# Kernel tuning notes

Hardware: AMD Instinct MI355X
Metric: run time of the kernel (lower is better)

## Reference

```python
import math
import jax, jax.numpy as jnp
import numpy as np

EPS = 1e-5
NUM_HEADER = 2


def pos_encoding(C, T, dtype):
    i = jnp.arange(C)
    exp = -((i - (i % 2)).astype(dtype) / C)
    freqs = jnp.power(jnp.asarray(10000.0, dtype), exp)[:, None]      # [C,1]
    phases = ((i % 2).astype(dtype) * (np.pi / 2))[:, None]           # [C,1]
    pos = jnp.arange(T, dtype=dtype)[None, :]                         # [1,T]
    return jnp.sin(pos * freqs + phases)                              # [C,T]


def layernorm2d(x, g, b):
    # LayerNorm over (C,T) jointly, per batch element (nn.LayerNorm([C, length]))
    mu = jnp.mean(x, axis=(1, 2), keepdims=True)
    var = jnp.mean((x - mu) ** 2, axis=(1, 2), keepdims=True)
    return (x - mu) * jax.lax.rsqrt(var + EPS) * g[None] + b[None]


def dsconv(x, dw_w, dw_b, pw_w, pw_b):
    # depthwise conv1d (groups=C, 'same' padding for odd k) + pointwise 1x1
    C = x.shape[1]
    k = dw_w.shape[-1]
    y = jax.lax.conv_general_dilated(
        x, dw_w[:, None, :], (1,), [(k // 2, k // 2)],
        dimension_numbers=('NCH', 'OIH', 'NCH'), feature_group_count=C)
    y = y + dw_b[None, :, None]
    y = jnp.einsum('bct,oc->bot', y, pw_w) + pw_b[None, :, None]
    return y


def attention(x, mask, Wq, Wk, Wv, Wo):
    # Faithful to source bug: all heads use Wqs[1]/Wks[1]/Wvs[1] -> identical heads.
    xt = jnp.transpose(x, (0, 2, 1))          # [B,T,C]
    C = xt.shape[-1]
    dk = C / NUM_HEADER
    q = xt @ Wq                               # [B,T,dk]
    k_ = xt @ Wk
    v = xt @ Wv
    s = jnp.einsum('bqd,bkd->bqk', q, k_) * (1.0 / math.sqrt(dk))
    hmask = mask[:, None, :]                  # mask over keys
    s = s * hmask + (1 - hmask) * (-1e30)
    a = jax.nn.softmax(s, axis=2) * mask[:, :, None]
    head = a @ v                              # [B,T,dk]
    heads = jnp.tile(head, (1, 1, NUM_HEADER))  # concat of identical heads
    out = heads @ Wo                          # [B,T,C]
    return jnp.transpose(out, (0, 2, 1))      # [B,C,T]


def setup_inputs() -> dict:
    key = jax.random.key(0)
    B, C, T = 16, 128, 1024
    NCONV, K = 4, 7
    dk = C // NUM_HEADER
    ks = jax.random.split(key, 12)
    inp = {
        'x': jax.random.normal(ks[0], (B, C, T), jnp.float32),
        'mask': jnp.ones((B, T), jnp.float32),
        'dw_w': jax.random.normal(ks[1], (NCONV, C, K), jnp.float32) * math.sqrt(2.0 / K),
        'dw_b': jnp.zeros((NCONV, C), jnp.float32),
        'pw_w': jax.random.normal(ks[2], (NCONV, C, C), jnp.float32) * math.sqrt(2.0 / C),
        'pw_b': jnp.zeros((NCONV, C), jnp.float32),
        'norm0_g': jnp.ones((C, T), jnp.float32),
        'norm0_b': jnp.zeros((C, T), jnp.float32),
        'norms_g': jnp.ones((NCONV, C, T), jnp.float32),
        'norms_b': jnp.zeros((NCONV, C, T), jnp.float32),
        'norme_g': jnp.ones((C, T), jnp.float32),
        'norme_b': jnp.zeros((C, T), jnp.float32),
        'Wq': jax.random.normal(ks[3], (C, dk), jnp.float32) * math.sqrt(2.0 / (C + dk)),
        'Wk': jax.random.normal(ks[4], (C, dk), jnp.float32) * math.sqrt(2.0 / (C + dk)),
        'Wv': jax.random.normal(ks[5], (C, dk), jnp.float32) * math.sqrt(2.0 / (C + dk)),
        'Wo': jax.random.normal(ks[6], (C, C), jnp.float32) * math.sqrt(2.0 / C),
        'fc_w': jax.random.normal(ks[7], (C, C), jnp.float32) * (0.1 * math.sqrt(6.0 / (2 * C))),
        'fc_b': jnp.zeros((C,), jnp.float32),
    }
    return inp


def reference(x, mask, dw_w, dw_b, pw_w, pw_b, norm0_g, norm0_b,
              norms_g, norms_b, norme_g, norme_b,
              Wq, Wk, Wv, Wo, fc_w, fc_b):
    B, C, T = x.shape
    nconv = dw_w.shape[0]
    # dropout is identity in eval mode (reference is deterministic)
    out = x + pos_encoding(C, T, x.dtype)[None]
    res = layernorm2d(out, norm0_g, norm0_b)
    for i in range(nconv):
        out = dsconv(out, dw_w[i], dw_b[i], pw_w[i], pw_b[i])
        out = jax.nn.relu(out)
        out = out + res
        res = out
        out = layernorm2d(out, norms_g[i], norms_b[i])
    out = attention(out, mask, Wq, Wk, Wv, Wo)
    out = out + res
    res = out
    out = layernorm2d(out, norme_g, norme_b)
    out = jnp.einsum('bct,oc->bot', out, fc_w) + fc_b[None, :, None]
    out = jax.nn.relu(out)
    out = out + res
    return out
```

## Files before the change

kernel.cpp:

```cpp
#include <hip/hip_runtime.h>
#include <math.h>

#define BB 16
#define CC 128
#define TT 1024
#define KK 7
#define DK 64
#define NSPLIT 4

typedef float f32x4 __attribute__((ext_vector_type(4)));
typedef short s16x8 __attribute__((ext_vector_type(8)));

__device__ inline short f2bf(float f) {
  union { float f; unsigned u; } v; v.f = f;
  unsigned r = (v.u + 0x7FFFu + ((v.u >> 16) & 1u)) >> 16;
  return (short)r;
}

__device__ inline float bf2f(short s) {
  union { unsigned u; float f; } v;
  v.u = ((unsigned)(unsigned short)s) << 16;
  return v.f;
}

__device__ inline void block_partial_256(float s, float ss, float* dst) {
#pragma unroll
  for (int off = 32; off; off >>= 1) { s += __shfl_xor(s, off); ss += __shfl_xor(ss, off); }
  __shared__ float red[8];
  int w = threadIdx.x >> 6;
  if ((threadIdx.x & 63) == 0) { red[2 * w] = s; red[2 * w + 1] = ss; }
  __syncthreads();
  if (threadIdx.x == 0) {
    for (int i = 1; i < 4; ++i) { s += red[2 * i]; ss += red[2 * i + 1]; }
    dst[0] = s; dst[1] = ss;
  }
}

__device__ inline void ln_stats_from_parts(const float* part_batch, int n, float* sh) {
  if (threadIdx.x < 64) {
    float s = 0.f, ss = 0.f;
    for (int i = threadIdx.x; i < n; i += 64) { s += part_batch[2 * i]; ss += part_batch[2 * i + 1]; }
#pragma unroll
    for (int off = 32; off; off >>= 1) { s += __shfl_xor(s, off); ss += __shfl_xor(ss, off); }
    if (threadIdx.x == 0) {
      const float invN = 1.f / (float)(CC * TT);
      float mu = s * invN;
      sh[0] = mu;
      sh[1] = rsqrtf(ss * invN - mu * mu + 1e-5f);
    }
  }
  __syncthreads();
}

__global__ __launch_bounds__(256) void k_prep0(const float* __restrict__ pww,
                                               const float* __restrict__ Wq,
                                               const float* __restrict__ Wk,
                                               const float* __restrict__ Wv,
                                               const float* __restrict__ Wo,
                                               const float* __restrict__ fcw,
                                               const float* __restrict__ x,
                                               short* __restrict__ pwwb,
                                               short* __restrict__ wqkvb,
                                               short* __restrict__ wo2b,
                                               short* __restrict__ fcwb,
                                               float* __restrict__ part0) {
  if (blockIdx.x < 448) {
    int i = blockIdx.x * 256 + threadIdx.x;
    if (i < 65536) { pwwb[i] = f2bf(pww[i]); return; }
    i -= 65536;
    if (i < 24576) {
      int m = i >> 7, c = i & 127;
      int sel = m >> 6, d = m & 63;
      const float* srcp = sel == 0 ? Wq : (sel == 1 ? Wk : Wv);
      wqkvb[i] = f2bf(srcp[c * DK + d]);
      return;
    }
    i -= 24576;
    if (i < 8192) {
      int o = i >> 6, d = i & 63;
      wo2b[i] = f2bf(Wo[d * CC + o] + Wo[(d + 64) * CC + o]);
      return;
    }
    i -= 8192;
    fcwb[i] = f2bf(fcw[i]);
    return;
  }
  int w = threadIdx.x >> 6, lane = threadIdx.x & 63;
  int bc = (blockIdx.x - 448) * 4 + w;
  int c = bc & (CC - 1);
  float freq = expf(-((float)(c & ~1) * (1.f / (float)CC)) * 9.210340371976184f);
  float ph = (c & 1) ? 1.5707963267948966f : 0.f;
  const float* xr = x + (size_t)bc * TT;
  float s = 0.f, ss = 0.f;
#pragma unroll
  for (int k = 0; k < 4; ++k) {
    int t = (k * 64 + lane) * 4;
    float4 v = *(const float4*)(xr + t);
    v.x += sinf((float)(t + 0) * freq + ph);
    v.y += sinf((float)(t + 1) * freq + ph);
    v.z += sinf((float)(t + 2) * freq + ph);
    v.w += sinf((float)(t + 3) * freq + ph);
    s += v.x + v.y + v.z + v.w;
    ss += v.x * v.x + v.y * v.y + v.z * v.z + v.w * v.w;
  }
#pragma unroll
  for (int off = 32; off; off >>= 1) { s += __shfl_xor(s, off); ss += __shfl_xor(ss, off); }
  if (lane == 0) { part0[(size_t)bc * 2] = s; part0[(size_t)bc * 2 + 1] = ss; }
}

template <bool LN_IN, bool LN_RES, bool ADD_POS>
__global__ __launch_bounds__(256) void k_dsconv(const float* __restrict__ in,
                                                const float* __restrict__ lng,
                                                const float* __restrict__ lnb,
                                                const float* __restrict__ part_in, int npart,
                                                const float* __restrict__ dww,
                                                const float* __restrict__ dwb,
                                                const short* __restrict__ pwwb,
                                                const float* __restrict__ pwb,
                                                float* __restrict__ out,
                                                float* __restrict__ part_out) {
  int tile = blockIdx.x & 31, b = blockIdx.x >> 5;
  int t0 = tile * 32;
  __shared__ float stats[2];
  __shared__ float xs[CC][41];
  __shared__ float xr2[CC][33];
  __shared__ __align__(16) short Dt[32][136];
  ln_stats_from_parts(part_in + (size_t)b * npart * 2, npart, stats);
  float mu = stats[0], rs = stats[1];

  for (int i = threadIdx.x; i < CC * 10; i += 256) {
    int c = i / 10, q = i - c * 10;
    int tb = t0 - 4 + q * 4;
    const float* rowp = in + ((size_t)b * CC + c) * TT;
    float freq = 0.f, ph = 0.f;
    if (ADD_POS) {
      freq = expf(-((float)(c & ~1) * (1.f / (float)CC)) * 9.210340371976184f);
      ph = (c & 1) ? 1.5707963267948966f : 0.f;
    }
    float r0, r1, r2, r3, o0, o1, o2, o3;
    bool full = (tb >= 0) && (tb + 4 <= TT);
    if (full) {
      float4 v = *(const float4*)(rowp + tb);
      if (ADD_POS) {
        v.x += sinf((float)(tb + 0) * freq + ph);
        v.y += sinf((float)(tb + 1) * freq + ph);
        v.z += sinf((float)(tb + 2) * freq + ph);
        v.w += sinf((float)(tb + 3) * freq + ph);
      }
      r0 = v.x; r1 = v.y; r2 = v.z; r3 = v.w;
      o0 = r0; o1 = r1; o2 = r2; o3 = r3;
      if (LN_IN) {
        float4 g = *(const float4*)(lng + (size_t)c * TT + tb);
        float4 bv = *(const float4*)(lnb + (size_t)c * TT + tb);
        o0 = (r0 - mu) * rs * g.x + bv.x;
        o1 = (r1 - mu) * rs * g.y + bv.y;
        o2 = (r2 - mu) * rs * g.z + bv.z;
        o3 = (r3 - mu) * rs * g.w + bv.w;
      }
    } else {
      float rr[4], oo[4];
#pragma unroll
      for (int k = 0; k < 4; ++k) {
        int t = tb + k;
        bool inb = (t >= 0) && (t < TT);
        float rv = 0.f;
        if (inb) {
          rv = rowp[t];
          if (ADD_POS) rv += sinf((float)t * freq + ph);
        }
        rr[k] = rv;
        float ov = rv;
        if (LN_IN && inb)
          ov = (rv - mu) * rs * lng[(size_t)c * TT + t] + lnb[(size_t)c * TT + t];
        oo[k] = ov;
      }
      r0 = rr[0]; r1 = rr[1]; r2 = rr[2]; r3 = rr[3];
      o0 = oo[0]; o1 = oo[1]; o2 = oo[2]; o3 = oo[3];
    }
    if (LN_IN && q >= 1 && q <= 8) {
      int tl = (q - 1) * 4;
      xr2[c][tl] = r0; xr2[c][tl + 1] = r1; xr2[c][tl + 2] = r2; xr2[c][tl + 3] = r3;
    }
    int base = q * 4;
    xs[c][base] = o0; xs[c][base + 1] = o1; xs[c][base + 2] = o2; xs[c][base + 3] = o3;
  }
  __syncthreads();
  for (int i = threadIdx.x; i < 32 * CC; i += 256) {
    int t = i >> 7, c = i & 127;
    float a = dwb[c];
#pragma unroll
    for (int j = 0; j < KK; ++j) a += dww[c * KK + j] * xs[c][t + j + 1];
    Dt[t][c] = f2bf(a);
  }
  __syncthreads();

  int w = threadIdx.x >> 6, lane = threadIdx.x & 63;
  int lo = lane & 15, hi = lane >> 4;
  f32x4 acc[2][2];
#pragma unroll
  for (int mt = 0; mt < 2; ++mt)
#pragma unroll
    for (int nt = 0; nt < 2; ++nt) { acc[mt][nt][0] = 0.f; acc[mt][nt][1] = 0.f; acc[mt][nt][2] = 0.f; acc[mt][nt][3] = 0.f; }
#pragma unroll
  for (int ks = 0; ks < 4; ++ks) {
    s16x8 b0 = *(const s16x8*)&Dt[lo][ks * 32 + hi * 8];
    s16x8 b1 = *(const s16x8*)&Dt[16 + lo][ks * 32 + hi * 8];
    s16x8 a0 = *(const s16x8*)&pwwb[(size_t)(w * 32 + lo) * CC + ks * 32 + hi * 8];
    s16x8 a1 = *(const s16x8*)&pwwb[(size_t)(w * 32 + 16 + lo) * CC + ks * 32 + hi * 8];
    acc[0][0] = __builtin_amdgcn_mfma_f32_16x16x32_bf16(a0, b0, acc[0][0], 0, 0, 0);
    acc[0][1] = __builtin_amdgcn_mfma_f32_16x16x32_bf16(a0, b1, acc[0][1], 0, 0, 0);
    acc[1][0] = __builtin_amdgcn_mfma_f32_16x16x32_bf16(a1, b0, acc[1][0], 0, 0, 0);
    acc[1][1] = __builtin_amdgcn_mfma_f32_16x16x32_bf16(a1, b1, acc[1][1], 0, 0, 0);
  }

  float s = 0.f, ss = 0.f;
#pragma unroll
  for (int mt = 0; mt < 2; ++mt)
#pragma unroll
    for (int nt = 0; nt < 2; ++nt)
#pragma unroll
      for (int r = 0; r < 4; ++r) {
        int row = w * 32 + mt * 16 + hi * 4 + r;
        int tl = nt * 16 + lo;
        int t = t0 + tl;
        float v = acc[mt][nt][r] + pwb[row];
        v = v > 0.f ? v : 0.f;
        float rv;
        if (LN_RES) {
          float raw = xs[row][tl + 4];
          rv = (raw - mu) * rs * lng[row * TT + t] + lnb[row * TT + t];
        } else if (LN_IN) {
          rv = xr2[row][tl];
        } else {
          rv = xs[row][tl + 4];
        }
        v += rv;
        xr2[row][tl] = v;
        s += v; ss += v * v;
      }
  __syncthreads();
  for (int u = threadIdx.x; u < 1024; u += 256) {
    int c = u >> 3, q = u & 7;
    float4 o4;
    o4.x = xr2[c][q * 4]; o4.y = xr2[c][q * 4 + 1];
    o4.z = xr2[c][q * 4 + 2]; o4.w = xr2[c][q * 4 + 3];
    *(float4*)(out + ((size_t)b * CC + c) * TT + t0 + q * 4) = o4;
  }
  block_partial_256(s, ss, part_out + (size_t)blockIdx.x * 2);
}

__global__ __launch_bounds__(256) void k_qkv(const float* __restrict__ in,
                                             const float* __restrict__ lng,
                                             const float* __restrict__ lnb,
                                             const float* __restrict__ part_in,
                                             const short* __restrict__ wqkvb,
                                             short* __restrict__ q,
                                             short* __restrict__ k,
                                             short* __restrict__ vt) {
  int tile = blockIdx.x & 31, b = blockIdx.x >> 5;
  int t0 = tile * 32;
  __shared__ float stats[2];
  __shared__ __align__(16) short Dt[32][136];
  __shared__ __align__(16) short stgQ[32 * 64];
  __shared__ __align__(16) short stgK[32 * 64];
  __shared__ __align__(16) short stgV[64][40];
  ln_stats_from_parts(part_in + (size_t)b * 64, 32, stats);
  float mu = stats[0], rs = stats[1];
  for (int i = threadIdx.x; i < CC * 8; i += 256) {
    int c = i >> 3, qq = i & 7;
    int t = qq * 4;
    size_t off = (size_t)c * TT + t0 + t;
    float4 v = *(const float4*)(in + (size_t)b * CC * TT + off);
    float4 g = *(const float4*)(lng + off);
    float4 bb = *(const float4*)(lnb + off);
    Dt[t + 0][c] = f2bf((v.x - mu) * rs * g.x + bb.x);
    Dt[t + 1][c] = f2bf((v.y - mu) * rs * g.y + bb.y);
    Dt[t + 2][c] = f2bf((v.z - mu) * rs * g.z + bb.z);
    Dt[t + 3][c] = f2bf((v.w - mu) * rs * g.w + bb.w);
  }
  __syncthreads();

  int w = threadIdx.x >> 6, lane = threadIdx.x & 63;
  int lo = lane & 15, hi = lane >> 4;
  f32x4 acc[3][2];
#pragma unroll
  for (int mt = 0; mt < 3; ++mt)
#pragma unroll
    for (int nt = 0; nt < 2; ++nt) { acc[mt][nt][0] = 0.f; acc[mt][nt][1] = 0.f; acc[mt][nt][2] = 0.f; acc[mt][nt][3] = 0.f; }
#pragma unroll
  for (int ks = 0; ks < 4; ++ks) {
    s16x8 b0 = *(const s16x8*)&Dt[lo][ks * 32 + hi * 8];
    s16x8 b1 = *(const s16x8*)&Dt[16 + lo][ks * 32 + hi * 8];
#pragma unroll
    for (int mt = 0; mt < 3; ++mt) {
      s16x8 a = *(const s16x8*)&wqkvb[(size_t)(w * 48 + mt * 16 + lo) * CC + ks * 32 + hi * 8];
      acc[mt][0] = __builtin_amdgcn_mfma_f32_16x16x32_bf16(a, b0, acc[mt][0], 0, 0, 0);
      acc[mt][1] = __builtin_amdgcn_mfma_f32_16x16x32_bf16(a, b1, acc[mt][1], 0, 0, 0);
    }
  }
#pragma unroll
  for (int mt = 0; mt < 3; ++mt)
#pragma unroll
    for (int nt = 0; nt < 2; ++nt) {
      int m0 = w * 48 + mt * 16 + hi * 4;
      int tl = nt * 16 + lo;
      short pv[4];
#pragma unroll
      for (int j = 0; j < 4; ++j) pv[j] = f2bf(acc[mt][nt][j]);
      if (m0 < 64) {
        *(short4*)&stgQ[tl * 64 + m0] = make_short4(pv[0], pv[1], pv[2], pv[3]);
      } else if (m0 < 128) {
        *(short4*)&stgK[tl * 64 + (m0 - 64)] = make_short4(pv[0], pv[1], pv[2], pv[3]);
      } else {
        int d = m0 - 128;
#pragma unroll
        for (int j = 0; j < 4; ++j) stgV[d + j][tl] = pv[j];
      }
    }
  __syncthreads();
  {
    int t = threadIdx.x >> 3, ch = threadIdx.x & 7;
    *(s16x8*)(q + ((size_t)b * TT + t0 + t) * DK + ch * 8) = *(const s16x8*)&stgQ[t * 64 + ch * 8];
    *(s16x8*)(k + ((size_t)b * TT + t0 + t) * DK + ch * 8) = *(const s16x8*)&stgK[t * 64 + ch * 8];
    int d = threadIdx.x >> 2, cv = threadIdx.x & 3;
    *(s16x8*)(vt + ((size_t)b * DK + d) * TT + t0 + cv * 8) = *(const s16x8*)&stgV[d][cv * 8];
  }
}

__global__ __launch_bounds__(128) void k_attn(const short* __restrict__ qb,
                                              const short* __restrict__ kbuf,
                                              const short* __restrict__ vtb,
                                              const float* __restrict__ mask,
                                              short* __restrict__ pacch,
                                              float* __restrict__ pml) {
  int sp = blockIdx.x & (NSPLIT - 1);
  int qt = (blockIdx.x >> 2) & 31;
  int b = blockIdx.x >> 7;
  int w = threadIdx.x >> 6, lane = threadIdx.x & 63;
  int lo = lane & 15, hi = lane >> 4;

  __shared__ __align__(16) short ks[64][72];
  __shared__ __align__(16) short vt[64][72];
  __shared__ __align__(16) short ps[2][16][68];
  __shared__ float ms[64];

  const short* qp = qb + ((size_t)b * TT + qt * 32 + w * 16 + lo) * DK + hi * 8;
  s16x8 aq0 = *(const s16x8*)qp;
  s16x8 aq1 = *(const s16x8*)(qp + 32);

  f32x4 acc[4];
  float m_i[4], l_i[4];
#pragma unroll
  for (int r = 0; r < 4; ++r) {
    m_i[r] = -3.0e38f; l_i[r] = 0.f;
#pragma unroll
    for (int nt = 0; nt < 4; ++nt) acc[nt][r] = 0.f;
  }
  const float scale = 0.125f;

  for (int kb2 = sp * (TT / 64 / NSPLIT); kb2 < (sp + 1) * (TT / 64 / NSPLIT); ++kb2) {
    __syncthreads();
    for (int i = threadIdx.x; i < 512; i += 128) {
      int r = i >> 3, ch = i & 7;
      *(s16x8*)&ks[r][ch * 8] =
          *(const s16x8*)(kbuf + ((size_t)b * TT + kb2 * 64 + r) * DK + ch * 8);
      *(s16x8*)&vt[r][ch * 8] =
          *(const s16x8*)(vtb + ((size_t)b * DK + r) * TT + kb2 * 64 + ch * 8);
    }
    if (threadIdx.x < 64) ms[threadIdx.x] = mask[(size_t)b * TT + kb2 * 64 + threadIdx.x];
    __syncthreads();

    f32x4 sc[4];
#pragma unroll
    for (int nt = 0; nt < 4; ++nt) {
      f32x4 z; z[0] = 0.f; z[1] = 0.f; z[2] = 0.f; z[3] = 0.f;
      s16x8 bk0 = *(const s16x8*)&ks[nt * 16 + lo][hi * 8];
      s16x8 bk1 = *(const s16x8*)&ks[nt * 16 + lo][32 + hi * 8];
      z = __builtin_amdgcn_mfma_f32_16x16x32_bf16(aq0, bk0, z, 0, 0, 0);
      z = __builtin_amdgcn_mfma_f32_16x16x32_bf16(aq1, bk1, z, 0, 0, 0);
      sc[nt] = z;
    }
#pragma unroll
    for (int nt = 0; nt < 4; ++nt) {
      float mv = ms[nt * 16 + lo];
      float addv = (1.f - mv) * -1e30f;
#pragma unroll
      for (int r = 0; r < 4; ++r) sc[nt][r] = sc[nt][r] * scale * mv + addv;
    }
    float alpha[4];
#pragma unroll
    for (int r = 0; r < 4; ++r) {
      float m0 = fmaxf(fmaxf(sc[0][r], sc[1][r]), fmaxf(sc[2][r], sc[3][r]));
#pragma unroll
      for (int off = 1; off < 16; off <<= 1) m0 = fmaxf(m0, __shfl_xor(m0, off));
      float mn = fmaxf(m_i[r], m0);
      alpha[r] = __expf(m_i[r] - mn);
      m_i[r] = mn;
    }
    float psum[4] = {0.f, 0.f, 0.f, 0.f};
#pragma unroll
    for (int nt = 0; nt < 4; ++nt)
#pragma unroll
      for (int r = 0; r < 4; ++r) {
        float p = __expf(sc[nt][r] - m_i[r]);
        psum[r] += p;
        ps[w][hi * 4 + r][nt * 16 + lo] = f2bf(p);
      }
#pragma unroll
    for (int r = 0; r < 4; ++r) {
      float sum = psum[r];
#pragma unroll
      for (int off = 1; off < 16; off <<= 1) sum += __shfl_xor(sum, off);
      l_i[r] = l_i[r] * alpha[r] + sum;
    }
#pragma unroll
    for (int nt = 0; nt < 4; ++nt)
#pragma unroll
      for (int r = 0; r < 4; ++r) acc[nt][r] *= alpha[r];

    s16x8 ap0 = *(const s16x8*)&ps[w][lo][hi * 8];
    s16x8 ap1 = *(const s16x8*)&ps[w][lo][32 + hi * 8];
#pragma unroll
    for (int nt = 0; nt < 4; ++nt) {
      s16x8 bv0 = *(const s16x8*)&vt[nt * 16 + lo][hi * 8];
      s16x8 bv1 = *(const s16x8*)&vt[nt * 16 + lo][32 + hi * 8];
      acc[nt] = __builtin_amdgcn_mfma_f32_16x16x32_bf16(ap0, bv0, acc[nt], 0, 0, 0);
      acc[nt] = __builtin_amdgcn_mfma_f32_16x16x32_bf16(ap1, bv1, acc[nt], 0, 0, 0);
    }
  }
  __syncthreads();
  short* pc = &ks[0][0];
#pragma unroll
  for (int r = 0; r < 4; ++r) {
    int row = w * 16 + hi * 4 + r;
#pragma unroll
    for (int nt = 0; nt < 4; ++nt) pc[row * 64 + nt * 16 + lo] = f2bf(acc[nt][r]);
    if (lo == 0) {
      size_t mb = (((size_t)b * TT + qt * 32 + row) * NSPLIT + sp) * 2;
      pml[mb] = m_i[r];
      pml[mb + 1] = l_i[r];
    }
  }
  __syncthreads();
  for (int u = threadIdx.x; u < 256; u += 128) {
    int row = u >> 3, ch = u & 7;
    size_t pb = (((size_t)b * TT + qt * 32 + row) * NSPLIT + sp) * DK;
    *(s16x8*)(pacch + pb + ch * 8) = *(const s16x8*)&pc[row * 64 + ch * 8];
  }
}

__global__ __launch_bounds__(256) void k_attnout2(const short* __restrict__ pacch,
                                                  const float* __restrict__ pml,
                                                  const float* __restrict__ mask,
                                                  const short* __restrict__ wo2b,
                                                  const float* __restrict__ res,
                                                  float* __restrict__ out,
                                                  float* __restrict__ part_out) {
  int tile = blockIdx.x & 31, b = blockIdx.x >> 5;
  int t0 = tile * 32;
  __shared__ __align__(16) short Ht[32][72];
  __shared__ float ot[128][33];
  {
    int i = threadIdx.x;
    int tr = i >> 3, q = i & 7;
    size_t rb = (size_t)b * TT + t0 + tr;
    float m[NSPLIT], l[NSPLIT];
#pragma unroll
    for (int s = 0; s < NSPLIT; ++s) {
      m[s] = pml[(rb * NSPLIT + s) * 2];
      l[s] = pml[(rb * NSPLIT + s) * 2 + 1];
    }
    float M = fmaxf(fmaxf(m[0], m[1]), fmaxf(m[2], m[3]));
    float wgt[NSPLIT], L = 0.f;
#pragma unroll
    for (int s = 0; s < NSPLIT; ++s) { wgt[s] = __expf(m[s] - M); L += wgt[s] * l[s]; }
    float inv = mask[rb] / L;
    float o[8] = {0.f, 0.f, 0.f, 0.f, 0.f, 0.f, 0.f, 0.f};
#pragma unroll
    for (int s = 0; s < NSPLIT; ++s) {
      s16x8 pv = *(const s16x8*)(pacch + (rb * NSPLIT + s) * DK + q * 8);
#pragma unroll
      for (int j = 0; j < 8; ++j) o[j] += wgt[s] * bf2f(pv[j]);
    }
    short h[8];
#pragma unroll
    for (int j = 0; j < 8; ++j) h[j] = f2bf(o[j] * inv);
    *(s16x8*)&Ht[tr][q * 8] = *(const s16x8*)h;
  }
  __syncthreads();

  int w = threadIdx.x >> 6, lane = threadIdx.x & 63;
  int lo = lane & 15, hi = lane >> 4;
  f32x4 acc[2][2];
#pragma unroll
  for (int mt = 0; mt < 2; ++mt)
#pragma unroll
    for (int nt = 0; nt < 2; ++nt) { acc[mt][nt][0] = 0.f; acc[mt][nt][1] = 0.f; acc[mt][nt][2] = 0.f; acc[mt][nt][3] = 0.f; }
#pragma unroll
  for (int ks = 0; ks < 2; ++ks) {
    s16x8 b0 = *(const s16x8*)&Ht[lo][ks * 32 + hi * 8];
    s16x8 b1 = *(const s16x8*)&Ht[16 + lo][ks * 32 + hi * 8];
    s16x8 a0 = *(const s16x8*)&wo2b[(size_t)(w * 32 + lo) * DK + ks * 32 + hi * 8];
    s16x8 a1 = *(const s16x8*)&wo2b[(size_t)(w * 32 + 16 + lo) * DK + ks * 32 + hi * 8];
    acc[0][0] = __builtin_amdgcn_mfma_f32_16x16x32_bf16(a0, b0, acc[0][0], 0, 0, 0);
    acc[0][1] = __builtin_amdgcn_mfma_f32_16x16x32_bf16(a0, b1, acc[0][1], 0, 0, 0);
    acc[1][0] = __builtin_amdgcn_mfma_f32_16x16x32_bf16(a1, b0, acc[1][0], 0, 0, 0);
    acc[1][1] = __builtin_amdgcn_mfma_f32_16x16x32_bf16(a1, b1, acc[1][1], 0, 0, 0);
  }
  float s = 0.f, ss = 0.f;
#pragma unroll
  for (int mt = 0; mt < 2; ++mt)
#pragma unroll
    for (int nt = 0; nt < 2; ++nt)
#pragma unroll
      for (int r = 0; r < 4; ++r) {
        int row = w * 32 + mt * 16 + hi * 4 + r;
        int tl = nt * 16 + lo;
        size_t idx = ((size_t)b * CC + row) * TT + t0 + tl;
        float v = acc[mt][nt][r] + res[idx];
        ot[row][tl] = v;
        s += v; ss += v * v;
      }
  __syncthreads();
  for (int u = threadIdx.x; u < 1024; u += 256) {
    int c = u >> 3, q = u & 7;
    float4 o4;
    o4.x = ot[c][q * 4]; o4.y = ot[c][q * 4 + 1];
    o4.z = ot[c][q * 4 + 2]; o4.w = ot[c][q * 4 + 3];
    *(float4*)(out + ((size_t)b * CC + c) * TT + t0 + q * 4) = o4;
  }
  block_partial_256(s, ss, part_out + (size_t)blockIdx.x * 2);
}

__global__ __launch_bounds__(256) void k_fc(const float* __restrict__ in,
                                            const float* __restrict__ lng,
                                            const float* __restrict__ lnb,
                                            const float* __restrict__ part_in,
                                            const short* __restrict__ fcwb,
                                            const float* __restrict__ fb,
                                            float* __restrict__ out) {
  int tile = blockIdx.x & 31, b = blockIdx.x >> 5;
  int t0 = tile * 32;
  __shared__ float stats[2];
  __shared__ float xr2[CC][33];
  __shared__ __align__(16) short Dt[32][136];
  ln_stats_from_parts(part_in + (size_t)b * 64, 32, stats);
  float mu = stats[0], rs = stats[1];
  for (int i = threadIdx.x; i < CC * 8; i += 256) {
    int c = i >> 3, q = i & 7;
    int t = q * 4;
    size_t off = (size_t)c * TT + t0 + t;
    float4 v = *(const float4*)(in + (size_t)b * CC * TT + off);
    float4 g = *(const float4*)(lng + off);
    float4 bb = *(const float4*)(lnb + off);
    xr2[c][t] = v.x; xr2[c][t + 1] = v.y; xr2[c][t + 2] = v.z; xr2[c][t + 3] = v.w;
    Dt[t + 0][c] = f2bf((v.x - mu) * rs * g.x + bb.x);
    Dt[t + 1][c] = f2bf((v.y - mu) * rs * g.y + bb.y);
    Dt[t + 2][c] = f2bf((v.z - mu) * rs * g.z + bb.z);
    Dt[t + 3][c] = f2bf((v.w - mu) * rs * g.w + bb.w);
  }
  __syncthreads();

  int w = threadIdx.x >> 6, lane = threadIdx.x & 63;
  int lo = lane & 15, hi = lane >> 4;
  f32x4 acc[2][2];
#pragma unroll
  for (int mt = 0; mt < 2; ++mt)
#pragma unroll
    for (int nt = 0; nt < 2; ++nt) { acc[mt][nt][0] = 0.f; acc[mt][nt][1] = 0.f; acc[mt][nt][2] = 0.f; acc[mt][nt][3] = 0.f; }
#pragma unroll
  for (int ks = 0; ks < 4; ++ks) {
    s16x8 b0 = *(const s16x8*)&Dt[lo][ks * 32 + hi * 8];
    s16x8 b1 = *(const s16x8*)&Dt[16 + lo][ks * 32 + hi * 8];
    s16x8 a0 = *(const s16x8*)&fcwb[(size_t)(w * 32 + lo) * CC + ks * 32 + hi * 8];
    s16x8 a1 = *(const s16x8*)&fcwb[(size_t)(w * 32 + 16 + lo) * CC + ks * 32 + hi * 8];
    acc[0][0] = __builtin_amdgcn_mfma_f32_16x16x32_bf16(a0, b0, acc[0][0], 0, 0, 0);
    acc[0][1] = __builtin_amdgcn_mfma_f32_16x16x32_bf16(a0, b1, acc[0][1], 0, 0, 0);
    acc[1][0] = __builtin_amdgcn_mfma_f32_16x16x32_bf16(a1, b0, acc[1][0], 0, 0, 0);
    acc[1][1] = __builtin_amdgcn_mfma_f32_16x16x32_bf16(a1, b1, acc[1][1], 0, 0, 0);
  }
#pragma unroll
  for (int mt = 0; mt < 2; ++mt)
#pragma unroll
    for (int nt = 0; nt < 2; ++nt)
#pragma unroll
      for (int r = 0; r < 4; ++r) {
        int row = w * 32 + mt * 16 + hi * 4 + r;
        int tl = nt * 16 + lo;
        float v = acc[mt][nt][r] + fb[row];
        v = v > 0.f ? v : 0.f;
        xr2[row][tl] = v + xr2[row][tl];
      }
  __syncthreads();
  for (int u = threadIdx.x; u < 1024; u += 256) {
    int c = u >> 3, q = u & 7;
    float4 o4;
    o4.x = xr2[c][q * 4]; o4.y = xr2[c][q * 4 + 1];
    o4.z = xr2[c][q * 4 + 2]; o4.w = xr2[c][q * 4 + 3];
    *(float4*)(out + ((size_t)b * CC + c) * TT + t0 + q * 4) = o4;
  }
}

extern "C" void kernel_launch(void* const* d_in, const int* in_sizes, int n_in,
                              void* d_out, int out_size, void* d_ws, size_t ws_size,
                              hipStream_t stream) {
  const float* x    = (const float*)d_in[0];
  const float* mask = (const float*)d_in[1];
  const float* dww  = (const float*)d_in[2];
  const float* dwb  = (const float*)d_in[3];
  const float* pww  = (const float*)d_in[4];
  const float* pwb  = (const float*)d_in[5];
  const float* n0g  = (const float*)d_in[6];
  const float* n0b  = (const float*)d_in[7];
  const float* nsg  = (const float*)d_in[8];
  const float* nsb  = (const float*)d_in[9];
  const float* neg_ = (const float*)d_in[10];
  const float* neb  = (const float*)d_in[11];
  const float* Wq   = (const float*)d_in[12];
  const float* Wk   = (const float*)d_in[13];
  const float* Wv   = (const float*)d_in[14];
  const float* Wo   = (const float*)d_in[15];
  const float* fcw  = (const float*)d_in[16];
  const float* fcb  = (const float*)d_in[17];
  float* out = (float*)d_out;

  float* W = (float*)d_ws;
  const size_t NBCT = (size_t)BB * CC * TT;
  const size_t NBTD = (size_t)BB * TT * DK;
  const size_t CT = (size_t)CC * TT;
  float* O     = W;
  float* S     = W + NBCT;
  float* PART0 = W + 2 * NBCT;
  float* PARTS = PART0 + 4096;
  float* PML   = PARTS + 5 * 1024;
  short* QB    = (short*)(PML + (size_t)BB * TT * NSPLIT * 2);
  short* KB    = QB + NBTD;
  short* VT    = KB + NBTD;
  short* PACCH = VT + NBTD;
  short* PWWB  = PACCH + NBTD * NSPLIT;
  short* WQKVB = PWWB + 65536;
  short* WO2B  = WQKVB + 24576;
  short* FCWB  = WO2B + 8192;

  k_prep0<<<960, 256, 0, stream>>>(pww, Wq, Wk, Wv, Wo, fcw, x,
                                   PWWB, WQKVB, WO2B, FCWB, PART0);
  k_dsconv<false, true, true><<<BB * 32, 256, 0, stream>>>(
      x, n0g, n0b, PART0, 128, dww, dwb, PWWB, pwb, S, PARTS);
  k_dsconv<true, false, false><<<BB * 32, 256, 0, stream>>>(
      S, nsg + 0 * CT, nsb + 0 * CT, PARTS, 32,
      dww + 1 * CC * KK, dwb + 1 * CC, PWWB + 1 * CC * CC, pwb + 1 * CC, O, PARTS + 1024);
  k_dsconv<true, false, false><<<BB * 32, 256, 0, stream>>>(
      O, nsg + 1 * CT, nsb + 1 * CT, PARTS + 1024, 32,
      dww + 2 * CC * KK, dwb + 2 * CC, PWWB + 2 * CC * CC, pwb + 2 * CC, S, PARTS + 2048);
  k_dsconv<true, false, false><<<BB * 32, 256, 0, stream>>>(
      S, nsg + 2 * CT, nsb + 2 * CT, PARTS + 2048, 32,
      dww + 3 * CC * KK, dwb + 3 * CC, PWWB + 3 * CC * CC, pwb + 3 * CC, O, PARTS + 3072);
  k_qkv<<<BB * 32, 256, 0, stream>>>(O, nsg + 3 * CT, nsb + 3 * CT, PARTS + 3072,
                                     WQKVB, QB, KB, VT);
  k_attn<<<BB * 32 * NSPLIT, 128, 0, stream>>>(QB, KB, VT, mask, PACCH, PML);
  k_attnout2<<<BB * 32, 256, 0, stream>>>(PACCH, PML, mask, WO2B, O, S, PARTS + 4096);
  k_fc<<<BB * 32, 256, 0, stream>>>(S, neg_, neb, PARTS + 4096, FCWB, fcb, out);
}
```

Baseline: 192.7 us.

## Halve time-tile width to double block count and prefetch attention K/V

Halves the time tile from 32 to 16 columns in the dsconv, qkv, attnout and fc kernels, which doubles the grid to 1024 blocks and shrinks the shared-memory footprint and accumulators. The aim is more parallelism and occupancy on the many compute units. The cost is a larger share of conv halo reloads per tile and twice as many LayerNorm partial sums. The attention kernel now prefetches the next K/V block into registers while the current block is computed, and attnout hoists its split-partial loads ahead of use.

```diff
diff --git a/kernel.cpp b/kernel.cpp
--- a/kernel.cpp
+++ b/kernel.cpp
@@ -7,6 +7,8 @@
 #define KK 7
 #define DK 64
 #define NSPLIT 4
+#define TW 16
+#define TNUM (TT / TW)
 
 typedef float f32x4 __attribute__((ext_vector_type(4)));
 typedef short s16x8 __attribute__((ext_vector_type(8)));
@@ -119,17 +121,17 @@
                                                 const float* __restrict__ pwb,
                                                 float* __restrict__ out,
                                                 float* __restrict__ part_out) {
-  int tile = blockIdx.x & 31, b = blockIdx.x >> 5;
-  int t0 = tile * 32;
+  int tile = blockIdx.x & (TNUM - 1), b = blockIdx.x >> 6;
+  int t0 = tile * TW;
   __shared__ float stats[2];
-  __shared__ float xs[CC][41];
-  __shared__ float xr2[CC][33];
-  __shared__ __align__(16) short Dt[32][136];
+  __shared__ float xs[CC][25];
+  __shared__ float xr2[CC][17];
+  __shared__ __align__(16) short Dt[TW][136];
   ln_stats_from_parts(part_in + (size_t)b * npart * 2, npart, stats);
   float mu = stats[0], rs = stats[1];
 
-  for (int i = threadIdx.x; i < CC * 10; i += 256) {
-    int c = i / 10, q = i - c * 10;
+  for (int i = threadIdx.x; i < CC * 6; i += 256) {
+    int c = i / 6, q = i - c * 6;
     int tb = t0 - 4 + q * 4;
     const float* rowp = in + ((size_t)b * CC + c) * TT;
     float freq = 0.f, ph = 0.f;
@@ -177,7 +179,7 @@
       r0 = rr[0]; r1 = rr[1]; r2 = rr[2]; r3 = rr[3];
       o0 = oo[0]; o1 = oo[1]; o2 = oo[2]; o3 = oo[3];
     }
-    if (LN_IN && q >= 1 && q <= 8) {
+    if (LN_IN && q >= 1 && q <= 4) {
       int tl = (q - 1) * 4;
       xr2[c][tl] = r0; xr2[c][tl + 1] = r1; xr2[c][tl + 2] = r2; xr2[c][tl + 3] = r3;
     }
@@ -185,7 +187,7 @@
     xs[c][base] = o0; xs[c][base + 1] = o1; xs[c][base + 2] = o2; xs[c][base + 3] = o3;
   }
   __syncthreads();
-  for (int i = threadIdx.x; i < 32 * CC; i += 256) {
+  for (int i = threadIdx.x; i < TW * CC; i += 256) {
     int t = i >> 7, c = i & 127;
     float a = dwb[c];
 #pragma unroll
@@ -196,51 +198,44 @@
 
   int w = threadIdx.x >> 6, lane = threadIdx.x & 63;
   int lo = lane & 15, hi = lane >> 4;
-  f32x4 acc[2][2];
-#pragma unroll
-  for (int mt = 0; mt < 2; ++mt)
-#pragma unroll
-    for (int nt = 0; nt < 2; ++nt) { acc[mt][nt][0] = 0.f; acc[mt][nt][1] = 0.f; acc[mt][nt][2] = 0.f; acc[mt][nt][3] = 0.f; }
+  f32x4 acc[2];
+#pragma unroll
+  for (int mt = 0; mt < 2; ++mt) { acc[mt][0] = 0.f; acc[mt][1] = 0.f; acc[mt][2] = 0.f; acc[mt][3] = 0.f; }
 #pragma unroll
   for (int ks = 0; ks < 4; ++ks) {
     s16x8 b0 = *(const s16x8*)&Dt[lo][ks * 32 + hi * 8];
-    s16x8 b1 = *(const s16x8*)&Dt[16 + lo][ks * 32 + hi * 8];
     s16x8 a0 = *(const s16x8*)&pwwb[(size_t)(w * 32 + lo) * CC + ks * 32 + hi * 8];
     s16x8 a1 = *(const s16x8*)&pwwb[(size_t)(w * 32 + 16 + lo) * CC + ks * 32 + hi * 8];
-    acc[0][0] = __builtin_amdgcn_mfma_f32_16x16x32_bf16(a0, b0, acc[0][0], 0, 0, 0);
-    acc[0][1] = __builtin_amdgcn_mfma_f32_16x16x32_bf16(a0, b1, acc[0][1], 0, 0, 0);
-    acc[1][0] = __builtin_amdgcn_mfma_f32_16x16x32_bf16(a1, b0, acc[1][0], 0, 0, 0);
-    acc[1][1] = __builtin_amdgcn_mfma_f32_16x16x32_bf16(a1, b1, acc[1][1], 0, 0, 0);
+    acc[0] = __builtin_amdgcn_mfma_f32_16x16x32_bf16(a0, b0, acc[0], 0, 0, 0);
+    acc[1] = __builtin_amdgcn_mfma_f32_16x16x32_bf16(a1, b0, acc[1], 0, 0, 0);
   }
 
   float s = 0.f, ss = 0.f;
 #pragma unroll
   for (int mt = 0; mt < 2; ++mt)
 #pragma unroll
-    for (int nt = 0; nt < 2; ++nt)
-#pragma unroll
-      for (int r = 0; r < 4; ++r) {
-        int row = w * 32 + mt * 16 + hi * 4 + r;
-        int tl = nt * 16 + lo;
-        int t = t0 + tl;
-        float v = acc[mt][nt][r] + pwb[row];
-        v = v > 0.f ? v : 0.f;
-        float rv;
-        if (LN_RES) {
-          float raw = xs[row][tl + 4];
-          rv = (raw - mu) * rs * lng[row * TT + t] + lnb[row * TT + t];
-        } else if (LN_IN) {
-          rv = xr2[row][tl];
-        } else {
-          rv = xs[row][tl + 4];
-        }
-        v += rv;
-        xr2[row][tl] = v;
-        s += v; ss += v * v;
+    for (int r = 0; r < 4; ++r) {
+      int row = w * 32 + mt * 16 + hi * 4 + r;
+      int tl = lo;
+      int t = t0 + tl;
+      float v = acc[mt][r] + pwb[row];
+      v = v > 0.f ? v : 0.f;
+      float rv;
+      if (LN_RES) {
+        float raw = xs[row][tl + 4];
+        rv = (raw - mu) * rs * lng[row * TT + t] + lnb[row * TT + t];
+      } else if (LN_IN) {
+        rv = xr2[row][tl];
+      } else {
+        rv = xs[row][tl + 4];
       }
-  __syncthreads();
-  for (int u = threadIdx.x; u < 1024; u += 256) {
-    int c = u >> 3, q = u & 7;
+      v += rv;
+      xr2[row][tl] = v;
+      s += v; ss += v * v;
+    }
+  __syncthreads();
+  for (int u = threadIdx.x; u < 512; u += 256) {
+    int c = u >> 2, q = u & 3;
     float4 o4;
     o4.x = xr2[c][q * 4]; o4.y = xr2[c][q * 4 + 1];
     o4.z = xr2[c][q * 4 + 2]; o4.w = xr2[c][q * 4 + 3];
@@ -257,17 +252,17 @@
                                              short* __restrict__ q,
                                              short* __restrict__ k,
                                              short* __restrict__ vt) {
-  int tile = blockIdx.x & 31, b = blockIdx.x >> 5;
-  int t0 = tile * 32;
+  int tile = blockIdx.x & (TNUM - 1), b = blockIdx.x >> 6;
+  int t0 = tile * TW;
   __shared__ float stats[2];
-  __shared__ __align__(16) short Dt[32][136];
-  __shared__ __align__(16) short stgQ[32 * 64];
-  __shared__ __align__(16) short stgK[32 * 64];
-  __shared__ __align__(16) short stgV[64][40];
-  ln_stats_from_parts(part_in + (size_t)b * 64, 32, stats);
+  __shared__ __align__(16) short Dt[TW][136];
+  __shared__ __align__(16) short stgQ[TW * 64];
+  __shared__ __align__(16) short stgK[TW * 64];
+  __shared__ __align__(16) short stgV[64][20];
+  ln_stats_from_parts(part_in + (size_t)b * 64 * 2, 64, stats);
   float mu = stats[0], rs = stats[1];
-  for (int i = threadIdx.x; i < CC * 8; i += 256) {
-    int c = i >> 3, qq = i & 7;
+  for (int i = threadIdx.x; i < CC * 4; i += 256) {
+    int c = i >> 2, qq = i & 3;
     int t = qq * 4;
     size_t off = (size_t)c * TT + t0 + t;
     float4 v = *(const float4*)(in + (size_t)b * CC * TT + off);
@@ -282,48 +277,46 @@
 
   int w = threadIdx.x >> 6, lane = threadIdx.x & 63;
   int lo = lane & 15, hi = lane >> 4;
-  f32x4 acc[3][2];
-#pragma unroll
-  for (int mt = 0; mt < 3; ++mt)
-#pragma unroll
-    for (int nt = 0; nt < 2; ++nt) { acc[mt][nt][0] = 0.f; acc[mt][nt][1] = 0.f; acc[mt][nt][2] = 0.f; acc[mt][nt][3] = 0.f; }
+  f32x4 acc[3];
+#pragma unroll
+  for (int mt = 0; mt < 3; ++mt) { acc[mt][0] = 0.f; acc[mt][1] = 0.f; acc[mt][2] = 0.f; acc[mt][3] = 0.f; }
 #pragma unroll
   for (int ks = 0; ks < 4; ++ks) {
     s16x8 b0 = *(const s16x8*)&Dt[lo][ks * 32 + hi * 8];
-    s16x8 b1 = *(const s16x8*)&Dt[16 + lo][ks * 32 + hi * 8];
 #pragma unroll
     for (int mt = 0; mt < 3; ++mt) {
       s16x8 a = *(const s16x8*)&wqkvb[(size_t)(w * 48 + mt * 16 + lo) * CC + ks * 32 + hi * 8];
-      acc[mt][0] = __builtin_amdgcn_mfma_f32_16x16x32_bf16(a, b0, acc[mt][0], 0, 0, 0);
-      acc[mt][1] = __builtin_amdgcn_mfma_f32_16x16x32_bf16(a, b1, acc[mt][1], 0, 0, 0);
-    }
-  }
-#pragma unroll
-  for (int mt = 0; mt < 3; ++mt)
-#pragma unroll
-    for (int nt = 0; nt < 2; ++nt) {
-      int m0 = w * 48 + mt * 16 + hi * 4;
-      int tl = nt * 16 + lo;
-      short pv[4];
-#pragma unroll
-      for (int j = 0; j < 4; ++j) pv[j] = f2bf(acc[mt][nt][j]);
-      if (m0 < 64) {
-        *(short4*)&stgQ[tl * 64 + m0] = make_short4(pv[0], pv[1], pv[2], pv[3]);
-      } else if (m0 < 128) {
-        *(short4*)&stgK[tl * 64 + (m0 - 64)] = make_short4(pv[0], pv[1], pv[2], pv[3]);
-      } else {
-        int d = m0 - 128;
-#pragma unroll
-        for (int j = 0; j < 4; ++j) stgV[d + j][tl] = pv[j];
-      }
-    }
+      acc[mt] = __builtin_amdgcn_mfma_f32_16x16x32_bf16(a, b0, acc[mt], 0, 0, 0);
+    }
+  }
+#pragma unroll
+  for (int mt = 0; mt < 3; ++mt) {
+    int m0 = w * 48 + mt * 16 + hi * 4;
+    int tl = lo;
+    short pv[4];
+#pragma unroll
+    for (int j = 0; j < 4; ++j) pv[j] = f2bf(acc[mt][j]);
+    if (m0 < 64) {
+      *(short4*)&stgQ[tl * 64 + m0] = make_short4(pv[0], pv[1], pv[2], pv[3]);
+    } else if (m0 < 128) {
+      *(short4*)&stgK[tl * 64 + (m0 - 64)] = make_short4(pv[0], pv[1], pv[2], pv[3]);
+    } else {
+      int d = m0 - 128;
+#pragma unroll
+      for (int j = 0; j < 4; ++j) stgV[d + j][tl] = pv[j];
+    }
+  }
   __syncthreads();
   {
-    int t = threadIdx.x >> 3, ch = threadIdx.x & 7;
-    *(s16x8*)(q + ((size_t)b * TT + t0 + t) * DK + ch * 8) = *(const s16x8*)&stgQ[t * 64 + ch * 8];
-    *(s16x8*)(k + ((size_t)b * TT + t0 + t) * DK + ch * 8) = *(const s16x8*)&stgK[t * 64 + ch * 8];
-    int d = threadIdx.x >> 2, cv = threadIdx.x & 3;
-    *(s16x8*)(vt + ((size_t)b * DK + d) * TT + t0 + cv * 8) = *(const s16x8*)&stgV[d][cv * 8];
+    int t = (threadIdx.x & 127) >> 3, ch = threadIdx.x & 7;
+    if (threadIdx.x < 128)
+      *(s16x8*)(q + ((size_t)b * TT + t0 + t) * DK + ch * 8) = *(const s16x8*)&stgQ[t * 64 + ch * 8];
+    else
+      *(s16x8*)(k + ((size_t)b * TT + t0 + t) * DK + ch * 8) = *(const s16x8*)&stgK[t * 64 + ch * 8];
+    if (threadIdx.x < 128) {
+      int d = threadIdx.x >> 1, cv = threadIdx.x & 1;
+      *(s16x8*)(vt + ((size_t)b * DK + d) * TT + t0 + cv * 8) = *(const s16x8*)&stgV[d][cv * 8];
+    }
   }
 }
 
@@ -357,18 +350,38 @@
     for (int nt = 0; nt < 4; ++nt) acc[nt][r] = 0.f;
   }
   const float scale = 0.125f;
-
-  for (int kb2 = sp * (TT / 64 / NSPLIT); kb2 < (sp + 1) * (TT / 64 / NSPLIT); ++kb2) {
+  const int kb0 = sp * (TT / 64 / NSPLIT);
+
+  s16x8 kreg[4], vreg[4];
+#pragma unroll
+  for (int j = 0; j < 4; ++j) {
+    int i = threadIdx.x + j * 128;
+    int r = i >> 3, ch = i & 7;
+    kreg[j] = *(const s16x8*)(kbuf + ((size_t)b * TT + kb0 * 64 + r) * DK + ch * 8);
+    vreg[j] = *(const s16x8*)(vtb + ((size_t)b * DK + r) * TT + kb0 * 64 + ch * 8);
+  }
+
+  for (int it = 0; it < 4; ++it) {
+    int kb2 = kb0 + it;
     __syncthreads();
-    for (int i = threadIdx.x; i < 512; i += 128) {
+#pragma unroll
+    for (int j = 0; j < 4; ++j) {
+      int i = threadIdx.x + j * 128;
       int r = i >> 3, ch = i & 7;
-      *(s16x8*)&ks[r][ch * 8] =
-          *(const s16x8*)(kbuf + ((size_t)b * TT + kb2 * 64 + r) * DK + ch * 8);
-      *(s16x8*)&vt[r][ch * 8] =
-          *(const s16x8*)(vtb + ((size_t)b * DK + r) * TT + kb2 * 64 + ch * 8);
+      *(s16x8*)&ks[r][ch * 8] = kreg[j];
+      *(s16x8*)&vt[r][ch * 8] = vreg[j];
     }
     if (threadIdx.x < 64) ms[threadIdx.x] = mask[(size_t)b * TT + kb2 * 64 + threadIdx.x];
     __syncthreads();
+    if (it < 3) {
+#pragma unroll
+      for (int j = 0; j < 4; ++j) {
+        int i = threadIdx.x + j * 128;
+        int r = i >> 3, ch = i & 7;
+        kreg[j] = *(const s16x8*)(kbuf + ((size_t)b * TT + (kb2 + 1) * 64 + r) * DK + ch * 8);
+        vreg[j] = *(const s16x8*)(vtb + ((size_t)b * DK + r) * TT + (kb2 + 1) * 64 + ch * 8);
+      }
+    }
 
     f32x4 sc[4];
 #pragma unroll
@@ -456,14 +469,18 @@
                                                   const float* __restrict__ res,
                                                   float* __restrict__ out,
                                                   float* __restrict__ part_out) {
-  int tile = blockIdx.x & 31, b = blockIdx.x >> 5;
-  int t0 = tile * 32;
-  __shared__ __align__(16) short Ht[32][72];
-  __shared__ float ot[128][33];
-  {
+  int tile = blockIdx.x & (TNUM - 1), b = blockIdx.x >> 6;
+  int t0 = tile * TW;
+  __shared__ __align__(16) short Ht[TW][72];
+  __shared__ float ot[CC][17];
+  if (threadIdx.x < 128) {
     int i = threadIdx.x;
     int tr = i >> 3, q = i & 7;
     size_t rb = (size_t)b * TT + t0 + tr;
+    s16x8 pvv[NSPLIT];
+#pragma unroll
+    for (int s = 0; s < NSPLIT; ++s)
+      pvv[s] = *(const s16x8*)(pacch + (rb * NSPLIT + s) * DK + q * 8);
     float m[NSPLIT], l[NSPLIT];
 #pragma unroll
     for (int s = 0; s < NSPLIT; ++s) {
@@ -478,9 +495,8 @@
     float o[8] = {0.f, 0.f, 0.f, 0.f, 0.f, 0.f, 0.f, 0.f};
 #pragma unroll
     for (int s = 0; s < NSPLIT; ++s) {
-      s16x8 pv = *(const s16x8*)(pacch + (rb * NSPLIT + s) * DK + q * 8);
-#pragma unroll
-      for (int j = 0; j < 8; ++j) o[j] += wgt[s] * bf2f(pv[j]);
+#pragma unroll
+      for (int j = 0; j < 8; ++j) o[j] += wgt[s] * bf2f(pvv[s][j]);
     }
     short h[8];
 #pragma unroll
@@ -491,39 +507,32 @@
 
   int w = threadIdx.x >> 6, lane = threadIdx.x & 63;
   int lo = lane & 15, hi = lane >> 4;
-  f32x4 acc[2][2];
-#pragma unroll
-  for (int mt = 0; mt < 2; ++mt)
-#pragma unroll
-    for (int nt = 0; nt < 2; ++nt) { acc[mt][nt][0] = 0.f; acc[mt][nt][1] = 0.f; acc[mt][nt][2] = 0.f; acc[mt][nt][3] = 0.f; }
+  f32x4 acc[2];
+#pragma unroll
+  for (int mt = 0; mt < 2; ++mt) { acc[mt][0] = 0.f; acc[mt][1] = 0.f; acc[mt][2] = 0.f; acc[mt][3] = 0.f; }
 #pragma unroll
   for (int ks = 0; ks < 2; ++ks) {
     s16x8 b0 = *(const s16x8*)&Ht[lo][ks * 32 + hi * 8];
-    s16x8 b1 = *(const s16x8*)&Ht[16 + lo][ks * 32 + hi * 8];
     s16x8 a0 = *(const s16x8*)&wo2b[(size_t)(w * 32 + lo) * DK + ks * 32 + hi * 8];
     s16x8 a1 = *(const s16x8*)&wo2b[(size_t)(w * 32 + 16 + lo) * DK + ks * 32 + hi * 8];
-    acc[0][0] = __builtin_amdgcn_mfma_f32_16x16x32_bf16(a0, b0, acc[0][0], 0, 0, 0);
-    acc[0][1] = __builtin_amdgcn_mfma_f32_16x16x32_bf16(a0, b1, acc[0][1], 0, 0, 0);
-    acc[1][0] = __builtin_amdgcn_mfma_f32_16x16x32_bf16(a1, b0, acc[1][0], 0, 0, 0);
-    acc[1][1] = __builtin_amdgcn_mfma_f32_16x16x32_bf16(a1, b1, acc[1][1], 0, 0, 0);
+    acc[0] = __builtin_amdgcn_mfma_f32_16x16x32_bf16(a0, b0, acc[0], 0, 0, 0);
+    acc[1] = __builtin_amdgcn_mfma_f32_16x16x32_bf16(a1, b0, acc[1], 0, 0, 0);
   }
   float s = 0.f, ss = 0.f;
 #pragma unroll
   for (int mt = 0; mt < 2; ++mt)
 #pragma unroll
-    for (int nt = 0; nt < 2; ++nt)
-#pragma unroll
-      for (int r = 0; r < 4; ++r) {
-        int row = w * 32 + mt * 16 + hi * 4 + r;
-        int tl = nt * 16 + lo;
-        size_t idx = ((size_t)b * CC + row) * TT + t0 + tl;
-        float v = acc[mt][nt][r] + res[idx];
-        ot[row][tl] = v;
-        s += v; ss += v * v;
-      }
-  __syncthreads();
-  for (int u = threadIdx.x; u < 1024; u += 256) {
-    int c = u >> 3, q = u & 7;
+    for (int r = 0; r < 4; ++r) {
+      int row = w * 32 + mt * 16 + hi * 4 + r;
+      int tl = lo;
+      size_t idx = ((size_t)b * CC + row) * TT + t0 + tl;
+      float v = acc[mt][r] + res[idx];
+      ot[row][tl] = v;
+      s += v; ss += v * v;
+    }
+  __syncthreads();
+  for (int u = threadIdx.x; u < 512; u += 256) {
+    int c = u >> 2, q = u & 3;
     float4 o4;
     o4.x = ot[c][q * 4]; o4.y = ot[c][q * 4 + 1];
     o4.z = ot[c][q * 4 + 2]; o4.w = ot[c][q * 4 + 3];
@@ -539,15 +548,15 @@
                                             const short* __restrict__ fcwb,
                                             const float* __restrict__ fb,
                                             float* __restrict__ out) {
-  int tile = blockIdx.x & 31, b = blockIdx.x >> 5;
-  int t0 = tile * 32;
+  int tile = blockIdx.x & (TNUM - 1), b = blockIdx.x >> 6;
+  int t0 = tile * TW;
   __shared__ float stats[2];
-  __shared__ float xr2[CC][33];
-  __shared__ __align__(16) short Dt[32][136];
-  ln_stats_from_parts(part_in + (size_t)b * 64, 32, stats);
+  __shared__ float xr2[CC][17];
+  __shared__ __align__(16) short Dt[TW][136];
+  ln_stats_from_parts(part_in + (size_t)b * 64 * 2, 64, stats);
   float mu = stats[0], rs = stats[1];
-  for (int i = threadIdx.x; i < CC * 8; i += 256) {
-    int c = i >> 3, q = i & 7;
+  for (int i = threadIdx.x; i < CC * 4; i += 256) {
+    int c = i >> 2, q = i & 3;
     int t = q * 4;
     size_t off = (size_t)c * TT + t0 + t;
     float4 v = *(const float4*)(in + (size_t)b * CC * TT + off);
@@ -563,37 +572,30 @@
 
   int w = threadIdx.x >> 6, lane = threadIdx.x & 63;
   int lo = lane & 15, hi = lane >> 4;
-  f32x4 acc[2][2];
-#pragma unroll
-  for (int mt = 0; mt < 2; ++mt)
-#pragma unroll
-    for (int nt = 0; nt < 2; ++nt) { acc[mt][nt][0] = 0.f; acc[mt][nt][1] = 0.f; acc[mt][nt][2] = 0.f; acc[mt][nt][3] = 0.f; }
+  f32x4 acc[2];
+#pragma unroll
+  for (int mt = 0; mt < 2; ++mt) { acc[mt][0] = 0.f; acc[mt][1] = 0.f; acc[mt][2] = 0.f; acc[mt][3] = 0.f; }
 #pragma unroll
   for (int ks = 0; ks < 4; ++ks) {
     s16x8 b0 = *(const s16x8*)&Dt[lo][ks * 32 + hi * 8];
-    s16x8 b1 = *(const s16x8*)&Dt[16 + lo][ks * 32 + hi * 8];
     s16x8 a0 = *(const s16x8*)&fcwb[(size_t)(w * 32 + lo) * CC + ks * 32 + hi * 8];
     s16x8 a1 = *(const s16x8*)&fcwb[(size_t)(w * 32 + 16 + lo) * CC + ks * 32 + hi * 8];
-    acc[0][0] = __builtin_amdgcn_mfma_f32_16x16x32_bf16(a0, b0, acc[0][0], 0, 0, 0);
-    acc[0][1] = __builtin_amdgcn_mfma_f32_16x16x32_bf16(a0, b1, acc[0][1], 0, 0, 0);
-    acc[1][0] = __builtin_amdgcn_mfma_f32_16x16x32_bf16(a1, b0, acc[1][0], 0, 0, 0);
-    acc[1][1] = __builtin_amdgcn_mfma_f32_16x16x32_bf16(a1, b1, acc[1][1], 0, 0, 0);
+    acc[0] = __builtin_amdgcn_mfma_f32_16x16x32_bf16(a0, b0, acc[0], 0, 0, 0);
+    acc[1] = __builtin_amdgcn_mfma_f32_16x16x32_bf16(a1, b0, acc[1], 0, 0, 0);
   }
 #pragma unroll
   for (int mt = 0; mt < 2; ++mt)
 #pragma unroll
-    for (int nt = 0; nt < 2; ++nt)
-#pragma unroll
-      for (int r = 0; r < 4; ++r) {
-        int row = w * 32 + mt * 16 + hi * 4 + r;
-        int tl = nt * 16 + lo;
-        float v = acc[mt][nt][r] + fb[row];
-        v = v > 0.f ? v : 0.f;
-        xr2[row][tl] = v + xr2[row][tl];
-      }
-  __syncthreads();
-  for (int u = threadIdx.x; u < 1024; u += 256) {
-    int c = u >> 3, q = u & 7;
+    for (int r = 0; r < 4; ++r) {
+      int row = w * 32 + mt * 16 + hi * 4 + r;
+      int tl = lo;
+      float v = acc[mt][r] + fb[row];
+      v = v > 0.f ? v : 0.f;
+      xr2[row][tl] = v + xr2[row][tl];
+    }
+  __syncthreads();
+  for (int u = threadIdx.x; u < 512; u += 256) {
+    int c = u >> 2, q = u & 3;
     float4 o4;
     o4.x = xr2[c][q * 4]; o4.y = xr2[c][q * 4 + 1];
     o4.z = xr2[c][q * 4 + 2]; o4.w = xr2[c][q * 4 + 3];
@@ -632,7 +634,7 @@
   float* S     = W + NBCT;
   float* PART0 = W + 2 * NBCT;
   float* PARTS = PART0 + 4096;
-  float* PML   = PARTS + 5 * 1024;
+  float* PML   = PARTS + 6 * 2048;
   short* QB    = (short*)(PML + (size_t)BB * TT * NSPLIT * 2);
   short* KB    = QB + NBTD;
   short* VT    = KB + NBTD;
@@ -644,20 +646,20 @@
 
   k_prep0<<<960, 256, 0, stream>>>(pww, Wq, Wk, Wv, Wo, fcw, x,
                                    PWWB, WQKVB, WO2B, FCWB, PART0);
-  k_dsconv<false, true, true><<<BB * 32, 256, 0, stream>>>(
+  k_dsconv<false, true, true><<<BB * TNUM, 256, 0, stream>>>(
       x, n0g, n0b, PART0, 128, dww, dwb, PWWB, pwb, S, PARTS);
-  k_dsconv<true, false, false><<<BB * 32, 256, 0, stream>>>(
-      S, nsg + 0 * CT, nsb + 0 * CT, PARTS, 32,
-      dww + 1 * CC * KK, dwb + 1 * CC, PWWB + 1 * CC * CC, pwb + 1 * CC, O, PARTS + 1024);
-  k_dsconv<true, false, false><<<BB * 32, 256, 0, stream>>>(
-      O, nsg + 1 * CT, nsb + 1 * CT, PARTS + 1024, 32,
-      dww + 2 * CC * KK, dwb + 2 * CC, PWWB + 2 * CC * CC, pwb + 2 * CC, S, PARTS + 2048);
-  k_dsconv<true, false, false><<<BB * 32, 256, 0, stream>>>(
-      S, nsg + 2 * CT, nsb + 2 * CT, PARTS + 2048, 32,
-      dww + 3 * CC * KK, dwb + 3 * CC, PWWB + 3 * CC * CC, pwb + 3 * CC, O, PARTS + 3072);
-  k_qkv<<<BB * 32, 256, 0, stream>>>(O, nsg + 3 * CT, nsb + 3 * CT, PARTS + 3072,
-                                     WQKVB, QB, KB, VT);
+  k_dsconv<true, false, false><<<BB * TNUM, 256, 0, stream>>>(
+      S, nsg + 0 * CT, nsb + 0 * CT, PARTS, 64,
+      dww + 1 * CC * KK, dwb + 1 * CC, PWWB + 1 * CC * CC, pwb + 1 * CC, O, PARTS + 2048);
+  k_dsconv<true, false, false><<<BB * TNUM, 256, 0, stream>>>(
+      O, nsg + 1 * CT, nsb + 1 * CT, PARTS + 2048, 64,
+      dww + 2 * CC * KK, dwb + 2 * CC, PWWB + 2 * CC * CC, pwb + 2 * CC, S, PARTS + 4096);
+  k_dsconv<true, false, false><<<BB * TNUM, 256, 0, stream>>>(
+      S, nsg + 2 * CT, nsb + 2 * CT, PARTS + 4096, 64,
+      dww + 3 * CC * KK, dwb + 3 * CC, PWWB + 3 * CC * CC, pwb + 3 * CC, O, PARTS + 6144);
+  k_qkv<<<BB * TNUM, 256, 0, stream>>>(O, nsg + 3 * CT, nsb + 3 * CT, PARTS + 6144,
+                                       WQKVB, QB, KB, VT);
   k_attn<<<BB * 32 * NSPLIT, 128, 0, stream>>>(QB, KB, VT, mask, PACCH, PML);
-  k_attnout2<<<BB * 32, 256, 0, stream>>>(PACCH, PML, mask, WO2B, O, S, PARTS + 4096);
-  k_fc<<<BB * 32, 256, 0, stream>>>(S, neg_, neb, PARTS + 4096, FCWB, fcb, out);
-}
+  k_attnout2<<<BB * TNUM, 256, 0, stream>>>(PACCH, PML, mask, WO2B, O, S, PARTS + 8192);
+  k_fc<<<BB * TNUM, 256, 0, stream>>>(S, neg_, neb, PARTS + 8192, FCWB, fcb, out);
+}
```

After: 208.2 us. 1.08x slower.
